# Kernel tuning notes

Measured on AMD Instinct MI355X. Metric: run time of the kernel, lower is better.

Reference implementation:

```python
import jax, jax.numpy as jnp
import numpy as np

N, E, D, L = 50000, 800000, 128, 3

def setup_inputs() -> dict:
    key = jax.random.key(0)
    ks = jax.random.split(key, 6)
    X = jax.random.normal(ks[0], (N, D), dtype=jnp.float32)
    edge_index = jax.random.randint(ks[1], (2, E), 0, N, dtype=jnp.int64)
    eps = jax.random.normal(ks[2], (L,), dtype=jnp.float32)
    # Glorot-ish scaling for stability
    W1 = jax.random.normal(ks[3], (L, D, D), dtype=jnp.float32) / np.sqrt(D)
    b1 = jnp.zeros((L, D), dtype=jnp.float32)
    W2 = jax.random.normal(ks[4], (L, D, D), dtype=jnp.float32) / np.sqrt(D)
    b2 = jnp.zeros((L, D), dtype=jnp.float32)
    return {"X": X, "edge_index": edge_index, "eps": eps,
            "W1": W1, "b1": b1, "W2": W2, "b2": b2}

def reference(X, edge_index, eps, W1, b1, W2, b2):
    src = edge_index[0]  # message sources j (flow source_to_target)
    dst = edge_index[1]  # aggregation targets i
    n = X.shape[0]
    for i in range(L):  # fixed small layer loop
        X0 = X
        # propagate: gather X_j over edges, scatter-add to targets
        S = jax.ops.segment_sum(X[src], dst, num_segments=n)  # [N, D]
        Z = (1.0 + eps[i]) * X + S
        # MLP: Linear -> ReLU -> Linear
        H = jnp.maximum(Z @ W1[i] + b1[i], 0.0)
        X = H @ W2[i] + b2[i]
        X = X + X0  # residual=True
    return X
```

## Files before the change

### kernel.cpp

```cpp
#include <hip/hip_runtime.h>

#define NN 50000
#define NE 800000
#define DD 128
#define NL 3
#define ELLW 64
#define MT_TOTAL (NN / 16)
#define MT_PER_XCD 391
#define NODES_PER_XCD (MT_PER_XCD * 16)
#define SCAT_BLKS (MT_PER_XCD * 8)
#define SCAT_CHUNK 2048
#define PACK_BLKS ((6 * 2048 + 255) / 256)
#define INIT_BLKS 3128

typedef short bf16x8 __attribute__((ext_vector_type(8)));
typedef float f32x4 __attribute__((ext_vector_type(4)));
typedef _Float16 half8 __attribute__((ext_vector_type(8)));
typedef unsigned short u16x8 __attribute__((ext_vector_type(8)));

__device__ __forceinline__ unsigned short f2bf(float x) {
  unsigned u = __float_as_uint(x);
  u += 0x7FFFu + ((u >> 16) & 1u);
  return (unsigned short)(u >> 16);
}
__device__ __forceinline__ float bf2f(unsigned short h) {
  return __uint_as_float(((unsigned)h) << 16);
}
__device__ __forceinline__ void cvt8(const float* zz, bf16x8* hi, bf16x8* lo) {
#pragma unroll
  for (int i = 0; i < 8; ++i) {
    unsigned short h = f2bf(zz[i]);
    (*hi)[i] = (short)h;
    (*lo)[i] = (short)f2bf(zz[i] - bf2f(h));
  }
}

__global__ __launch_bounds__(256) void prologue_k(
    const int* __restrict__ ei, int* __restrict__ cnt, unsigned short* __restrict__ ell,
    const float* __restrict__ W1, const float* __restrict__ W2,
    unsigned short* __restrict__ Wp,
    const float* __restrict__ X, _Float16* __restrict__ Xh)
{
  int b = blockIdx.x;
  if (b < SCAT_BLKS) {
    int g = b & 7, chunk = b >> 3;
    int lo = g * NODES_PER_XCD, hi = lo + NODES_PER_XCD;
    int base = chunk * SCAT_CHUNK + threadIdx.x * 8;
    if (base + 7 < NE) {
      int4 d0 = *(const int4*)(ei + NE + base);
      int4 d1 = *(const int4*)(ei + NE + base + 4);
      int4 s0 = *(const int4*)(ei + base);
      int4 s1 = *(const int4*)(ei + base + 4);
      int dd[8] = {d0.x, d0.y, d0.z, d0.w, d1.x, d1.y, d1.z, d1.w};
      int ss[8] = {s0.x, s0.y, s0.z, s0.w, s1.x, s1.y, s1.z, s1.w};
#pragma unroll
      for (int i = 0; i < 8; ++i) {
        int d = dd[i];
        if (d >= lo && d < hi) {
          int pos = atomicAdd(&cnt[d], 1);
          if (pos < ELLW) ell[(size_t)d * ELLW + pos] = (unsigned short)ss[i];
        }
      }
    } else {
      for (int e = base; e < NE; ++e) {
        int d = ei[NE + e];
        if (d >= lo && d < hi) {
          int pos = atomicAdd(&cnt[d], 1);
          if (pos < ELLW) ell[(size_t)d * ELLW + pos] = (unsigned short)ei[e];
        }
      }
    }
  } else if (b < SCAT_BLKS + PACK_BLKS) {
    int t = (b - SCAT_BLKS) * 256 + threadIdx.x;
    if (t < 6 * 2048) {
      int m = t >> 11;
      int rem = t & 2047;
      int l = rem & 63;
      int ntks = rem >> 6;
      int ks = ntks & 3, nt = ntks >> 2;
      const float* W = (m < 3) ? (W1 + (size_t)m * DD * DD) : (W2 + (size_t)(m - 3) * DD * DD);
      int col = nt * 16 + (l & 15);
      int k0 = ks * 32 + (l >> 4) * 8;
      unsigned short* hi = Wp + (size_t)m * 2 * DD * DD + (size_t)rem * 8;
      unsigned short* lo = hi + DD * DD;
#pragma unroll
      for (int i = 0; i < 8; ++i) {
        float w = W[(size_t)(k0 + i) * DD + col];
        unsigned short h = f2bf(w);
        hi[i] = h;
        lo[i] = f2bf(w - bf2f(h));
      }
    }
  } else {
    int bb = b - SCAT_BLKS - PACK_BLKS;
    int g = bb & 7, ii = bb >> 3;
    int mt = g * MT_PER_XCD + ii;
    if (mt < MT_TOTAL) {
      size_t base = (size_t)mt * 16 * DD + threadIdx.x * 8;
      const float4* p = (const float4*)(X + base);
      float4 a = p[0], bb2 = p[1];
      half8 h;
      h[0] = (_Float16)a.x;   h[1] = (_Float16)a.y;   h[2] = (_Float16)a.z;   h[3] = (_Float16)a.w;
      h[4] = (_Float16)bb2.x; h[5] = (_Float16)bb2.y; h[6] = (_Float16)bb2.z; h[7] = (_Float16)bb2.w;
      *(half8*)(Xh + base) = h;
    }
  }
}

__global__ __launch_bounds__(256) void sort_k(const int* __restrict__ cnt,
                                              int* __restrict__ perm) {
  __shared__ int lh[ELLW + 1];
  __shared__ int cur[ELLW + 1];
  int g = blockIdx.x;
  int base = g * NODES_PER_XCD;
  int nend = base + NODES_PER_XCD; if (nend > NN) nend = NN;
  for (int i = threadIdx.x; i <= ELLW; i += 256) lh[i] = 0;
  __syncthreads();
  for (int n = base + threadIdx.x; n < nend; n += 256) {
    int deg = cnt[n]; deg = deg > ELLW ? ELLW : deg;
    atomicAdd(&lh[deg], 1);
  }
  __syncthreads();
  if (threadIdx.x == 0) {
    int run = base;
    for (int b = 0; b <= ELLW; ++b) { cur[b] = run; run += lh[b]; }
  }
  __syncthreads();
  for (int n = base + threadIdx.x; n < nend; n += 256) {
    int deg = cnt[n]; deg = deg > ELLW ? ELLW : deg;
    int rank = atomicAdd(&cur[deg], 1);
    perm[rank] = n | (deg << 16);
  }
}

template<int OUT_F32>
__global__ __launch_bounds__(256) void fused_layer_k(
    const _Float16* __restrict__ Xh_in,
    const int* __restrict__ perm, const unsigned short* __restrict__ ell,
    const float* __restrict__ eps, int layer,
    const unsigned short* __restrict__ Wp1, const float* __restrict__ b1,
    const unsigned short* __restrict__ Wp2, const float* __restrict__ b2,
    float* __restrict__ Xf_out, _Float16* __restrict__ Xh_out)
{
  __shared__ float ztile[16 * 132];
  __shared__ unsigned short rtile[16 * 136];
  const int part = blockIdx.x & 7;
  const int ii = blockIdx.x >> 3;
  const int iis = (ii * 7) % MT_PER_XCD;
  const int mt = part * MT_PER_XCD + iis;
  if (mt >= MT_TOTAL) return;
  const int w = threadIdx.x >> 6, l = threadIdx.x & 63;
  const int c = l & 15, grp = l >> 4;

  {
    const float e1 = 1.0f + eps[layer];
    const int nl = w * 4 + grp;
    const int pe = perm[mt * 16 + nl];
    const int node = pe & 0xFFFF;
    const int deg = pe >> 16;
    const unsigned short* el = ell + (size_t)node * ELLW;
    const u16x8* el8 = (const u16x8*)el;
    half8 sv = *(const half8*)(Xh_in + (size_t)node * DD + c * 8);
    *(u16x8*)(rtile + nl * 136 + c * 8) = *(const u16x8*)&sv;
    half8 acch = (half8)(_Float16)0.0f;
    int nf8 = deg >> 3;
    u16x8 nxt;
    if (nf8) nxt = el8[0];
    for (int t = 0; t < nf8; ++t) {
      u16x8 cur = nxt;
      if (t + 1 < nf8) nxt = el8[t + 1];
      half8 v0 = *(const half8*)(Xh_in + (size_t)cur[0] * DD + c * 8);
      half8 v1 = *(const half8*)(Xh_in + (size_t)cur[1] * DD + c * 8);
      half8 v2 = *(const half8*)(Xh_in + (size_t)cur[2] * DD + c * 8);
      half8 v3 = *(const half8*)(Xh_in + (size_t)cur[3] * DD + c * 8);
      half8 v4 = *(const half8*)(Xh_in + (size_t)cur[4] * DD + c * 8);
      half8 v5 = *(const half8*)(Xh_in + (size_t)cur[5] * DD + c * 8);
      half8 v6 = *(const half8*)(Xh_in + (size_t)cur[6] * DD + c * 8);
      half8 v7 = *(const half8*)(Xh_in + (size_t)cur[7] * DD + c * 8);
      half8 s = ((v0 + v1) + (v2 + v3)) + ((v4 + v5) + (v6 + v7));
      acch += s;
    }
    for (int j = nf8 * 8; j < deg; ++j) {
      half8 v = *(const half8*)(Xh_in + (size_t)el[j] * DD + c * 8);
      acch += v;
    }
    float acc[8];
#pragma unroll
    for (int i = 0; i < 8; ++i) acc[i] = fmaf(e1, (float)sv[i], (float)acch[i]);
    float* dst = ztile + nl * 132 + c * 8;
    *(float4*)dst = make_float4(acc[0], acc[1], acc[2], acc[3]);
    *(float4*)(dst + 4) = make_float4(acc[4], acc[5], acc[6], acc[7]);
  }
  __syncthreads();

  f32x4 acc1[2];
#pragma unroll
  for (int nt = 0; nt < 2; ++nt) acc1[nt] = (f32x4){0.f, 0.f, 0.f, 0.f};
  {
    const float* arow = ztile + (l & 15) * 132;
    const unsigned short* Whi = Wp1;
    const unsigned short* Wlo = Wp1 + DD * DD;
#pragma unroll
    for (int ks = 0; ks < 4; ++ks) {
      const float* zp = arow + ks * 32 + grp * 8;
      float zz[8] = {zp[0], zp[1], zp[2], zp[3], zp[4], zp[5], zp[6], zp[7]};
      bf16x8 ahi, alo; cvt8(zz, &ahi, &alo);
#pragma unroll
      for (int nt = 0; nt < 2; ++nt) {
        int ntb = w * 2 + nt;
        size_t off = ((size_t)(ntb * 4 + ks) * 64 + l) * 8;
        bf16x8 bhi = *(const bf16x8*)(Whi + off);
        bf16x8 blo = *(const bf16x8*)(Wlo + off);
        acc1[nt] = __builtin_amdgcn_mfma_f32_16x16x32_bf16(ahi, bhi, acc1[nt], 0, 0, 0);
        acc1[nt] = __builtin_amdgcn_mfma_f32_16x16x32_bf16(ahi, blo, acc1[nt], 0, 0, 0);
        acc1[nt] = __builtin_amdgcn_mfma_f32_16x16x32_bf16(alo, bhi, acc1[nt], 0, 0, 0);
      }
    }
  }
  __syncthreads();

  {
#pragma unroll
    for (int nt = 0; nt < 2; ++nt) {
      int ntb = w * 2 + nt;
      float bv = b1[ntb * 16 + c];
#pragma unroll
      for (int r = 0; r < 4; ++r)
        ztile[(grp * 4 + r) * 132 + ntb * 16 + c] = fmaxf(acc1[nt][r] + bv, 0.f);
    }
  }
  __syncthreads();

  f32x4 acc2[2];
#pragma unroll
  for (int nt = 0; nt < 2; ++nt) acc2[nt] = (f32x4){0.f, 0.f, 0.f, 0.f};
  {
    const float* arow = ztile + (l & 15) * 132;
    const unsigned short* Whi = Wp2;
    const unsigned short* Wlo = Wp2 + DD * DD;
#pragma unroll
    for (int ks = 0; ks < 4; ++ks) {
      const float* hp = arow + ks * 32 + grp * 8;
      float hh[8] = {hp[0], hp[1], hp[2], hp[3], hp[4], hp[5], hp[6], hp[7]};
      bf16x8 ahi, alo; cvt8(hh, &ahi, &alo);
#pragma unroll
      for (int nt = 0; nt < 2; ++nt) {
        int ntb = w * 2 + nt;
        size_t off = ((size_t)(ntb * 4 + ks) * 64 + l) * 8;
        bf16x8 bhi = *(const bf16x8*)(Whi + off);
        bf16x8 blo = *(const bf16x8*)(Wlo + off);
        acc2[nt] = __builtin_amdgcn_mfma_f32_16x16x32_bf16(ahi, bhi, acc2[nt], 0, 0, 0);
        acc2[nt] = __builtin_amdgcn_mfma_f32_16x16x32_bf16(ahi, blo, acc2[nt], 0, 0, 0);
        acc2[nt] = __builtin_amdgcn_mfma_f32_16x16x32_bf16(alo, bhi, acc2[nt], 0, 0, 0);
      }
    }
#pragma unroll
    for (int nt = 0; nt < 2; ++nt) {
      int ntb = w * 2 + nt;
      int col = ntb * 16 + c;
      float bv = b2[col];
#pragma unroll
      for (int r = 0; r < 4; ++r) {
        int row = grp * 4 + r;
        int onode = perm[mt * 16 + row] & 0xFFFF;
        size_t idx = (size_t)onode * DD + col;
        unsigned short rb = rtile[row * 136 + col];
        float rv = (float)(*(_Float16*)&rb);
        float v = acc2[nt][r] + bv + rv;
        if (OUT_F32) Xf_out[idx] = v;
        else         Xh_out[idx] = (_Float16)v;
      }
    }
  }
}

extern "C" void kernel_launch(void* const* d_in, const int* in_sizes, int n_in,
                              void* d_out, int out_size, void* d_ws, size_t ws_size,
                              hipStream_t stream) {
  const float* X   = (const float*)d_in[0];
  const int*   ei  = (const int*)d_in[1];
  const float* eps = (const float*)d_in[2];
  const float* W1  = (const float*)d_in[3];
  const float* b1  = (const float*)d_in[4];
  const float* W2  = (const float*)d_in[5];
  const float* b2  = (const float*)d_in[6];
  float* Xout = (float*)d_out;

  char* ws = (char*)d_ws;
  size_t off = 0;
  int* cnt  = (int*)(ws + off); off += 256 * (((size_t)NN * 4 + 255) / 256);
  int* perm = (int*)(ws + off); off += 256 * (((size_t)(MT_PER_XCD * 8 * 16) * 4 + 255) / 256);
  unsigned short* ell = (unsigned short*)(ws + off); off += (size_t)NN * ELLW * 2;
  unsigned short* Wp  = (unsigned short*)(ws + off); off += (size_t)6 * 2 * DD * DD * 2;
  off = 256 * ((off + 255) / 256);
  _Float16* Xh0 = (_Float16*)(ws + off); off += (size_t)NN * DD * 2;
  _Float16* Xh1 = (_Float16*)(ws + off); off += (size_t)NN * DD * 2;

  hipMemsetAsync(cnt, 0, (size_t)NN * 4, stream);
  prologue_k<<<SCAT_BLKS + PACK_BLKS + INIT_BLKS, 256, 0, stream>>>(
      ei, cnt, ell, W1, W2, Wp, X, Xh0);
  sort_k<<<8, 256, 0, stream>>>(cnt, perm);

  const int fgrid = MT_PER_XCD * 8;
  fused_layer_k<0><<<fgrid, 256, 0, stream>>>(Xh0, perm, ell, eps, 0,
      Wp + (size_t)0 * 2 * DD * DD, b1 + 0 * DD,
      Wp + (size_t)3 * 2 * DD * DD, b2 + 0 * DD, nullptr, Xh1);
  fused_layer_k<0><<<fgrid, 256, 0, stream>>>(Xh1, perm, ell, eps, 1,
      Wp + (size_t)1 * 2 * DD * DD, b1 + 1 * DD,
      Wp + (size_t)4 * 2 * DD * DD, b2 + 1 * DD, nullptr, Xh0);
  fused_layer_k<1><<<fgrid, 256, 0, stream>>>(Xh0, perm, ell, eps, 2,
      Wp + (size_t)2 * 2 * DD * DD, b1 + 2 * DD,
      Wp + (size_t)5 * 2 * DD * DD, b2 + 2 * DD, Xout, nullptr);
}
```

Baseline: 186.8 us.

## Process two 16-node tiles per block to reuse weight loads and interleave gathers

Each block of the fused GIN layer kernel now handles a pair of 16-node tiles instead of one, which halves the grid. The neighbor gathers for both tiles are interleaved in one loop to raise memory-level parallelism, and each weight fragment loaded from global memory feeds MFMAs for both tiles. The cost is doubled LDS usage and higher register pressure, which may lower occupancy. Load imbalance inside a pair is handled with per-tile predicates.

```diff
diff --git a/kernel.cpp b/kernel.cpp
--- a/kernel.cpp
+++ b/kernel.cpp
@@ -8,6 +8,7 @@
 #define MT_TOTAL (NN / 16)
 #define MT_PER_XCD 391
 #define NODES_PER_XCD (MT_PER_XCD * 16)
+#define NPAIR 196
 #define SCAT_BLKS (MT_PER_XCD * 8)
 #define SCAT_CHUNK 2048
 #define PACK_BLKS ((6 * 2048 + 255) / 256)
@@ -142,78 +143,124 @@
     const unsigned short* __restrict__ Wp2, const float* __restrict__ b2,
     float* __restrict__ Xf_out, _Float16* __restrict__ Xh_out)
 {
-  __shared__ float ztile[16 * 132];
-  __shared__ unsigned short rtile[16 * 136];
+  __shared__ float ztile[2][16 * 132];
+  __shared__ unsigned short rtile[2][16 * 136];
   const int part = blockIdx.x & 7;
-  const int ii = blockIdx.x >> 3;
-  const int iis = (ii * 7) % MT_PER_XCD;
-  const int mt = part * MT_PER_XCD + iis;
-  if (mt >= MT_TOTAL) return;
+  const int pi = blockIdx.x >> 3;
+  const int pis = (pi * 5) % NPAIR;
+  const int iiA = pis * 2, iiB = pis * 2 + 1;
+  const int mtA = part * MT_PER_XCD + iiA;
+  const int mtB = part * MT_PER_XCD + iiB;
+  const bool vA = (iiA < MT_PER_XCD) && (mtA < MT_TOTAL);
+  const bool vB = (iiB < MT_PER_XCD) && (mtB < MT_TOTAL);
   const int w = threadIdx.x >> 6, l = threadIdx.x & 63;
   const int c = l & 15, grp = l >> 4;
+  const int nl = w * 4 + grp;
 
   {
     const float e1 = 1.0f + eps[layer];
-    const int nl = w * 4 + grp;
-    const int pe = perm[mt * 16 + nl];
-    const int node = pe & 0xFFFF;
-    const int deg = pe >> 16;
-    const unsigned short* el = ell + (size_t)node * ELLW;
-    const u16x8* el8 = (const u16x8*)el;
-    half8 sv = *(const half8*)(Xh_in + (size_t)node * DD + c * 8);
-    *(u16x8*)(rtile + nl * 136 + c * 8) = *(const u16x8*)&sv;
-    half8 acch = (half8)(_Float16)0.0f;
-    int nf8 = deg >> 3;
-    u16x8 nxt;
-    if (nf8) nxt = el8[0];
-    for (int t = 0; t < nf8; ++t) {
-      u16x8 cur = nxt;
-      if (t + 1 < nf8) nxt = el8[t + 1];
-      half8 v0 = *(const half8*)(Xh_in + (size_t)cur[0] * DD + c * 8);
-      half8 v1 = *(const half8*)(Xh_in + (size_t)cur[1] * DD + c * 8);
-      half8 v2 = *(const half8*)(Xh_in + (size_t)cur[2] * DD + c * 8);
-      half8 v3 = *(const half8*)(Xh_in + (size_t)cur[3] * DD + c * 8);
-      half8 v4 = *(const half8*)(Xh_in + (size_t)cur[4] * DD + c * 8);
-      half8 v5 = *(const half8*)(Xh_in + (size_t)cur[5] * DD + c * 8);
-      half8 v6 = *(const half8*)(Xh_in + (size_t)cur[6] * DD + c * 8);
-      half8 v7 = *(const half8*)(Xh_in + (size_t)cur[7] * DD + c * 8);
-      half8 s = ((v0 + v1) + (v2 + v3)) + ((v4 + v5) + (v6 + v7));
-      acch += s;
-    }
-    for (int j = nf8 * 8; j < deg; ++j) {
-      half8 v = *(const half8*)(Xh_in + (size_t)el[j] * DD + c * 8);
-      acch += v;
-    }
-    float acc[8];
-#pragma unroll
-    for (int i = 0; i < 8; ++i) acc[i] = fmaf(e1, (float)sv[i], (float)acch[i]);
-    float* dst = ztile + nl * 132 + c * 8;
-    *(float4*)dst = make_float4(acc[0], acc[1], acc[2], acc[3]);
-    *(float4*)(dst + 4) = make_float4(acc[4], acc[5], acc[6], acc[7]);
-  }
-  __syncthreads();
-
-  f32x4 acc1[2];
-#pragma unroll
-  for (int nt = 0; nt < 2; ++nt) acc1[nt] = (f32x4){0.f, 0.f, 0.f, 0.f};
+    int peA = vA ? perm[mtA * 16 + nl] : 0;
+    int peB = vB ? perm[mtB * 16 + nl] : 0;
+    int nodeA = peA & 0xFFFF, degA = peA >> 16;
+    int nodeB = peB & 0xFFFF, degB = peB >> 16;
+    const unsigned short* elA = ell + (size_t)nodeA * ELLW;
+    const unsigned short* elB = ell + (size_t)nodeB * ELLW;
+    const u16x8* elA8 = (const u16x8*)elA;
+    const u16x8* elB8 = (const u16x8*)elB;
+    half8 svA = *(const half8*)(Xh_in + (size_t)nodeA * DD + c * 8);
+    half8 svB = *(const half8*)(Xh_in + (size_t)nodeB * DD + c * 8);
+    *(u16x8*)(rtile[0] + nl * 136 + c * 8) = *(const u16x8*)&svA;
+    *(u16x8*)(rtile[1] + nl * 136 + c * 8) = *(const u16x8*)&svB;
+    half8 accA = (half8)(_Float16)0.0f;
+    half8 accB = (half8)(_Float16)0.0f;
+    int nfA = degA >> 3, nfB = degB >> 3;
+    int nf = nfA > nfB ? nfA : nfB;
+    u16x8 nxtA, nxtB;
+    if (nfA) nxtA = elA8[0];
+    if (nfB) nxtB = elB8[0];
+    for (int t = 0; t < nf; ++t) {
+      bool dA = t < nfA, dB = t < nfB;
+      half8 a0, a1, a2, a3, a4, a5, a6, a7;
+      half8 b0, b1h, b2h, b3, b4, b5, b6, b7;
+      u16x8 curA, curB;
+      if (dA) {
+        curA = nxtA;
+        if (t + 1 < nfA) nxtA = elA8[t + 1];
+        a0 = *(const half8*)(Xh_in + (size_t)curA[0] * DD + c * 8);
+        a1 = *(const half8*)(Xh_in + (size_t)curA[1] * DD + c * 8);
+        a2 = *(const half8*)(Xh_in + (size_t)curA[2] * DD + c * 8);
+        a3 = *(const half8*)(Xh_in + (size_t)curA[3] * DD + c * 8);
+        a4 = *(const half8*)(Xh_in + (size_t)curA[4] * DD + c * 8);
+        a5 = *(const half8*)(Xh_in + (size_t)curA[5] * DD + c * 8);
+        a6 = *(const half8*)(Xh_in + (size_t)curA[6] * DD + c * 8);
+        a7 = *(const half8*)(Xh_in + (size_t)curA[7] * DD + c * 8);
+      }
+      if (dB) {
+        curB = nxtB;
+        if (t + 1 < nfB) nxtB = elB8[t + 1];
+        b0  = *(const half8*)(Xh_in + (size_t)curB[0] * DD + c * 8);
+        b1h = *(const half8*)(Xh_in + (size_t)curB[1] * DD + c * 8);
+        b2h = *(const half8*)(Xh_in + (size_t)curB[2] * DD + c * 8);
+        b3  = *(const half8*)(Xh_in + (size_t)curB[3] * DD + c * 8);
+        b4  = *(const half8*)(Xh_in + (size_t)curB[4] * DD + c * 8);
+        b5  = *(const half8*)(Xh_in + (size_t)curB[5] * DD + c * 8);
+        b6  = *(const half8*)(Xh_in + (size_t)curB[6] * DD + c * 8);
+        b7  = *(const half8*)(Xh_in + (size_t)curB[7] * DD + c * 8);
+      }
+      if (dA) accA += ((a0 + a1) + (a2 + a3)) + ((a4 + a5) + (a6 + a7));
+      if (dB) accB += ((b0 + b1h) + (b2h + b3)) + ((b4 + b5) + (b6 + b7));
+    }
+    for (int j = nfA * 8; j < degA; ++j)
+      accA += *(const half8*)(Xh_in + (size_t)elA[j] * DD + c * 8);
+    for (int j = nfB * 8; j < degB; ++j)
+      accB += *(const half8*)(Xh_in + (size_t)elB[j] * DD + c * 8);
+    float za[8], zb[8];
+#pragma unroll
+    for (int i = 0; i < 8; ++i) {
+      za[i] = fmaf(e1, (float)svA[i], (float)accA[i]);
+      zb[i] = fmaf(e1, (float)svB[i], (float)accB[i]);
+    }
+    float* dA2 = ztile[0] + nl * 132 + c * 8;
+    float* dB2 = ztile[1] + nl * 132 + c * 8;
+    *(float4*)dA2       = make_float4(za[0], za[1], za[2], za[3]);
+    *(float4*)(dA2 + 4) = make_float4(za[4], za[5], za[6], za[7]);
+    *(float4*)dB2       = make_float4(zb[0], zb[1], zb[2], zb[3]);
+    *(float4*)(dB2 + 4) = make_float4(zb[4], zb[5], zb[6], zb[7]);
+  }
+  __syncthreads();
+
+  f32x4 acc1A[2], acc1B[2];
+#pragma unroll
+  for (int nt = 0; nt < 2; ++nt) {
+    acc1A[nt] = (f32x4){0.f, 0.f, 0.f, 0.f};
+    acc1B[nt] = (f32x4){0.f, 0.f, 0.f, 0.f};
+  }
   {
-    const float* arow = ztile + (l & 15) * 132;
+    const float* arowA = ztile[0] + (l & 15) * 132;
+    const float* arowB = ztile[1] + (l & 15) * 132;
     const unsigned short* Whi = Wp1;
     const unsigned short* Wlo = Wp1 + DD * DD;
 #pragma unroll
     for (int ks = 0; ks < 4; ++ks) {
-      const float* zp = arow + ks * 32 + grp * 8;
-      float zz[8] = {zp[0], zp[1], zp[2], zp[3], zp[4], zp[5], zp[6], zp[7]};
-      bf16x8 ahi, alo; cvt8(zz, &ahi, &alo);
+      const float* zpA = arowA + ks * 32 + grp * 8;
+      const float* zpB = arowB + ks * 32 + grp * 8;
+      float zzA[8] = {zpA[0], zpA[1], zpA[2], zpA[3], zpA[4], zpA[5], zpA[6], zpA[7]};
+      float zzB[8] = {zpB[0], zpB[1], zpB[2], zpB[3], zpB[4], zpB[5], zpB[6], zpB[7]};
+      bf16x8 ahiA, aloA, ahiB, aloB;
+      cvt8(zzA, &ahiA, &aloA);
+      cvt8(zzB, &ahiB, &aloB);
 #pragma unroll
       for (int nt = 0; nt < 2; ++nt) {
         int ntb = w * 2 + nt;
         size_t off = ((size_t)(ntb * 4 + ks) * 64 + l) * 8;
         bf16x8 bhi = *(const bf16x8*)(Whi + off);
         bf16x8 blo = *(const bf16x8*)(Wlo + off);
-        acc1[nt] = __builtin_amdgcn_mfma_f32_16x16x32_bf16(ahi, bhi, acc1[nt], 0, 0, 0);
-        acc1[nt] = __builtin_amdgcn_mfma_f32_16x16x32_bf16(ahi, blo, acc1[nt], 0, 0, 0);
-        acc1[nt] = __builtin_amdgcn_mfma_f32_16x16x32_bf16(alo, bhi, acc1[nt], 0, 0, 0);
+        acc1A[nt] = __builtin_amdgcn_mfma_f32_16x16x32_bf16(ahiA, bhi, acc1A[nt], 0, 0, 0);
+        acc1A[nt] = __builtin_amdgcn_mfma_f32_16x16x32_bf16(ahiA, blo, acc1A[nt], 0, 0, 0);
+        acc1A[nt] = __builtin_amdgcn_mfma_f32_16x16x32_bf16(aloA, bhi, acc1A[nt], 0, 0, 0);
+        acc1B[nt] = __builtin_amdgcn_mfma_f32_16x16x32_bf16(ahiB, bhi, acc1B[nt], 0, 0, 0);
+        acc1B[nt] = __builtin_amdgcn_mfma_f32_16x16x32_bf16(ahiB, blo, acc1B[nt], 0, 0, 0);
+        acc1B[nt] = __builtin_amdgcn_mfma_f32_16x16x32_bf16(aloB, bhi, acc1B[nt], 0, 0, 0);
       }
     }
   }
@@ -225,33 +272,46 @@
       int ntb = w * 2 + nt;
       float bv = b1[ntb * 16 + c];
 #pragma unroll
-      for (int r = 0; r < 4; ++r)
-        ztile[(grp * 4 + r) * 132 + ntb * 16 + c] = fmaxf(acc1[nt][r] + bv, 0.f);
-    }
-  }
-  __syncthreads();
-
-  f32x4 acc2[2];
-#pragma unroll
-  for (int nt = 0; nt < 2; ++nt) acc2[nt] = (f32x4){0.f, 0.f, 0.f, 0.f};
+      for (int r = 0; r < 4; ++r) {
+        ztile[0][(grp * 4 + r) * 132 + ntb * 16 + c] = fmaxf(acc1A[nt][r] + bv, 0.f);
+        ztile[1][(grp * 4 + r) * 132 + ntb * 16 + c] = fmaxf(acc1B[nt][r] + bv, 0.f);
+      }
+    }
+  }
+  __syncthreads();
+
+  f32x4 acc2A[2], acc2B[2];
+#pragma unroll
+  for (int nt = 0; nt < 2; ++nt) {
+    acc2A[nt] = (f32x4){0.f, 0.f, 0.f, 0.f};
+    acc2B[nt] = (f32x4){0.f, 0.f, 0.f, 0.f};
+  }
   {
-    const float* arow = ztile + (l & 15) * 132;
+    const float* arowA = ztile[0] + (l & 15) * 132;
+    const float* arowB = ztile[1] + (l & 15) * 132;
     const unsigned short* Whi = Wp2;
     const unsigned short* Wlo = Wp2 + DD * DD;
 #pragma unroll
     for (int ks = 0; ks < 4; ++ks) {
-      const float* hp = arow + ks * 32 + grp * 8;
-      float hh[8] = {hp[0], hp[1], hp[2], hp[3], hp[4], hp[5], hp[6], hp[7]};
-      bf16x8 ahi, alo; cvt8(hh, &ahi, &alo);
+      const float* hpA = arowA + ks * 32 + grp * 8;
+      const float* hpB = arowB + ks * 32 + grp * 8;
+      float hhA[8] = {hpA[0], hpA[1], hpA[2], hpA[3], hpA[4], hpA[5], hpA[6], hpA[7]};
+      float hhB[8] = {hpB[0], hpB[1], hpB[2], hpB[3], hpB[4], hpB[5], hpB[6], hpB[7]};
+      bf16x8 ahiA, aloA, ahiB, aloB;
+      cvt8(hhA, &ahiA, &aloA);
+      cvt8(hhB, &ahiB, &aloB);
 #pragma unroll
       for (int nt = 0; nt < 2; ++nt) {
         int ntb = w * 2 + nt;
         size_t off = ((size_t)(ntb * 4 + ks) * 64 + l) * 8;
         bf16x8 bhi = *(const bf16x8*)(Whi + off);
         bf16x8 blo = *(const bf16x8*)(Wlo + off);
-        acc2[nt] = __builtin_amdgcn_mfma_f32_16x16x32_bf16(ahi, bhi, acc2[nt], 0, 0, 0);
-        acc2[nt] = __builtin_amdgcn_mfma_f32_16x16x32_bf16(ahi, blo, acc2[nt], 0, 0, 0);
-        acc2[nt] = __builtin_amdgcn_mfma_f32_16x16x32_bf16(alo, bhi, acc2[nt], 0, 0, 0);
+        acc2A[nt] = __builtin_amdgcn_mfma_f32_16x16x32_bf16(ahiA, bhi, acc2A[nt], 0, 0, 0);
+        acc2A[nt] = __builtin_amdgcn_mfma_f32_16x16x32_bf16(ahiA, blo, acc2A[nt], 0, 0, 0);
+        acc2A[nt] = __builtin_amdgcn_mfma_f32_16x16x32_bf16(aloA, bhi, acc2A[nt], 0, 0, 0);
+        acc2B[nt] = __builtin_amdgcn_mfma_f32_16x16x32_bf16(ahiB, bhi, acc2B[nt], 0, 0, 0);
+        acc2B[nt] = __builtin_amdgcn_mfma_f32_16x16x32_bf16(ahiB, blo, acc2B[nt], 0, 0, 0);
+        acc2B[nt] = __builtin_amdgcn_mfma_f32_16x16x32_bf16(aloB, bhi, acc2B[nt], 0, 0, 0);
       }
     }
 #pragma unroll
@@ -262,13 +322,20 @@
 #pragma unroll
       for (int r = 0; r < 4; ++r) {
         int row = grp * 4 + r;
-        int onode = perm[mt * 16 + row] & 0xFFFF;
-        size_t idx = (size_t)onode * DD + col;
-        unsigned short rb = rtile[row * 136 + col];
-        float rv = (float)(*(_Float16*)&rb);
-        float v = acc2[nt][r] + bv + rv;
-        if (OUT_F32) Xf_out[idx] = v;
-        else         Xh_out[idx] = (_Float16)v;
+        if (vA) {
+          int onode = perm[mtA * 16 + row] & 0xFFFF;
+          size_t idx = (size_t)onode * DD + col;
+          unsigned short rb = rtile[0][row * 136 + col];
+          float v = acc2A[nt][r] + bv + (float)(*(_Float16*)&rb);
+          if (OUT_F32) Xf_out[idx] = v; else Xh_out[idx] = (_Float16)v;
+        }
+        if (vB) {
+          int onode = perm[mtB * 16 + row] & 0xFFFF;
+          size_t idx = (size_t)onode * DD + col;
+          unsigned short rb = rtile[1][row * 136 + col];
+          float v = acc2B[nt][r] + bv + (float)(*(_Float16*)&rb);
+          if (OUT_F32) Xf_out[idx] = v; else Xh_out[idx] = (_Float16)v;
+        }
       }
     }
   }
@@ -301,7 +368,7 @@
       ei, cnt, ell, W1, W2, Wp, X, Xh0);
   sort_k<<<8, 256, 0, stream>>>(cnt, perm);
 
-  const int fgrid = MT_PER_XCD * 8;
+  const int fgrid = NPAIR * 8;
   fused_layer_k<0><<<fgrid, 256, 0, stream>>>(Xh0, perm, ell, eps, 0,
       Wp + (size_t)0 * 2 * DD * DD, b1 + 0 * DD,
       Wp + (size_t)3 * 2 * DD * DD, b2 + 0 * DD, nullptr, Xh1);
```

After: 224.0 us. +19.9%, slower.
